# Optimization experiments

Measured on AMD Instinct MI355X. Metric: run time of the kernel, lower is better.

## Reference

```python
import jax, jax.numpy as jnp
from jax import lax
import numpy as np

N = 256          # HiPPO order
DT = 1.0 / 4096  # discretization step ~ 1/L
L = 4096         # sequence length
BATCH = 64


def _legt_transition(n):
    # LegT (translated Legendre) HiPPO transition matrices (continuous-time).
    Q = np.arange(n, dtype=np.float64)
    R = (2.0 * Q + 1.0) ** 0.5
    j, i = np.meshgrid(Q, Q)
    A = R[:, None] * np.where(i < j, (-1.0) ** (i - j), 1.0) * R[None, :]
    B = R[:, None]
    return -A, B


def _bilinear_discretize(A, B, dt):
    # scipy.signal.cont2discrete(..., method='bilinear')
    n = A.shape[0]
    I = np.eye(n)
    M = np.linalg.inv(I - (dt / 2.0) * A)
    Ad = M @ (I + (dt / 2.0) * A)
    Bd = (M @ B) * dt
    return Ad, Bd


def setup_inputs() -> dict:
    key = jax.random.key(0)
    A, B = _legt_transition(N)
    Ad, Bd = _bilinear_discretize(A, B, DT)
    inputs = jax.random.normal(key, (L, BATCH), dtype=jnp.float32)
    return {
        "inputs": inputs,
        "A": jnp.asarray(Ad, dtype=jnp.float32),          # (N, N)
        "B": jnp.asarray(Bd.squeeze(-1), dtype=jnp.float32),  # (N,)
    }


def reference(inputs, A, B):
    # inputs: (L, BATCH) -> output cs: (L, BATCH, N)
    u = inputs[..., None]  # (L, BATCH, 1)
    c0 = jnp.zeros((inputs.shape[1], A.shape[0]), dtype=inputs.dtype)  # (BATCH, N)

    def step(c, f):
        # c = F.linear(c, A) + B * f  ==  c @ A^T + B * f
        c = c @ A.T + B * f
        return c, c

    _, cs = lax.scan(step, c0, u)
    return cs
```

## Files before the change

### kernel.cpp

```cpp
#include <hip/hip_runtime.h>
#include <hip/hip_bf16.h>


#define MATF 65536

typedef __attribute__((ext_vector_type(8))) short short8;
typedef __attribute__((ext_vector_type(4))) float f32x4;

__device__ __forceinline__ unsigned short f2bf(float x) {
  union { __hip_bfloat16 h; unsigned short u; } cv;
  cv.h = __float2bfloat16(x);
  return cv.u;
}
__device__ __forceinline__ float bf2f(unsigned short u) {
  union { unsigned short u; __hip_bfloat16 h; } cv;
  cv.u = u;
  return __bfloat162float(cv.h);
}

__device__ __forceinline__ void load16_lds(const void* gsrc, void* ldst) {
  __builtin_amdgcn_global_load_lds(
      (const __attribute__((address_space(1))) unsigned int*)gsrc,
      (__attribute__((address_space(3))) unsigned int*)ldst,
      16, 0, 0);
}

__global__ __launch_bounds__(256) void gemm_nn_batch(
    const float* __restrict__ X, const float* __restrict__ Ys,
    float* __restrict__ Zs, int count)
{
  int g    = blockIdx.x >> 4;
  int tile = blockIdx.x & 15;
  if (g >= count) return;
  const float* Y = Ys + (size_t)g * MATF;
  float*       Z = Zs + (size_t)g * MATF;
  int tr = (tile >> 2) * 64;
  int tc = (tile & 3) * 64;

  __shared__ float As[64][33];
  __shared__ float Bs[32][65];
  int tid = threadIdx.x;
  int tx = tid & 15, ty = tid >> 4;
  float acc[4][4] = {};

  for (int k0 = 0; k0 < 256; k0 += 32) {
#pragma unroll
    for (int p = 0; p < 2; ++p) {
      int idx = tid + p * 256;
      int r = idx >> 3, c4 = (idx & 7) * 4;
      float4 v = *(const float4*)(X + (size_t)(tr + r) * 256 + k0 + c4);
      As[r][c4 + 0] = v.x; As[r][c4 + 1] = v.y; As[r][c4 + 2] = v.z; As[r][c4 + 3] = v.w;
    }
#pragma unroll
    for (int p = 0; p < 2; ++p) {
      int idx = tid + p * 256;
      int r = idx >> 4, c4 = (idx & 15) * 4;
      float4 v = *(const float4*)(Y + (size_t)(k0 + r) * 256 + tc + c4);
      Bs[r][c4 + 0] = v.x; Bs[r][c4 + 1] = v.y; Bs[r][c4 + 2] = v.z; Bs[r][c4 + 3] = v.w;
    }
    __syncthreads();
#pragma unroll
    for (int kk = 0; kk < 32; ++kk) {
      float a[4], b[4];
#pragma unroll
      for (int u = 0; u < 4; ++u) a[u] = As[ty * 4 + u][kk];
#pragma unroll
      for (int v = 0; v < 4; ++v) b[v] = Bs[kk][tx * 4 + v];
#pragma unroll
      for (int u = 0; u < 4; ++u)
#pragma unroll
        for (int v = 0; v < 4; ++v) acc[u][v] += a[u] * b[v];
    }
    __syncthreads();
  }
#pragma unroll
  for (int u = 0; u < 4; ++u)
#pragma unroll
    for (int v = 0; v < 4; ++v)
      Z[(size_t)(tr + ty * 4 + u) * 256 + tc + tx * 4 + v] = acc[u][v];
}

__global__ __launch_bounds__(256) void pow_first(
    const float* __restrict__ A, float* __restrict__ P)
{
  int bid = blockIdx.x, tid = threadIdx.x;
  if (bid >= 16) {
    int blk = bid - 16;
#pragma unroll
    for (int q = 0; q < 4; ++q) {
      int idx = blk * 1024 + q * 256 + tid;
      *(float4*)(P + (size_t)idx * 4) = *(const float4*)(A + (size_t)idx * 4);
    }
    return;
  }
  int tile = bid;
  int tr = (tile >> 2) * 64;
  int tc = (tile & 3) * 64;
  __shared__ float As[64][33];
  __shared__ float Bs[32][65];
  int tx = tid & 15, ty = tid >> 4;
  float acc[4][4] = {};
  for (int k0 = 0; k0 < 256; k0 += 32) {
#pragma unroll
    for (int p = 0; p < 2; ++p) {
      int idx = tid + p * 256;
      int r = idx >> 3, c4 = (idx & 7) * 4;
      float4 v = *(const float4*)(A + (size_t)(tr + r) * 256 + k0 + c4);
      As[r][c4 + 0] = v.x; As[r][c4 + 1] = v.y; As[r][c4 + 2] = v.z; As[r][c4 + 3] = v.w;
    }
#pragma unroll
    for (int p = 0; p < 2; ++p) {
      int idx = tid + p * 256;
      int r = idx >> 4, c4 = (idx & 15) * 4;
      float4 v = *(const float4*)(A + (size_t)(k0 + r) * 256 + tc + c4);
      Bs[r][c4 + 0] = v.x; Bs[r][c4 + 1] = v.y; Bs[r][c4 + 2] = v.z; Bs[r][c4 + 3] = v.w;
    }
    __syncthreads();
#pragma unroll
    for (int kk = 0; kk < 32; ++kk) {
      float a[4], b[4];
#pragma unroll
      for (int u = 0; u < 4; ++u) a[u] = As[ty * 4 + u][kk];
#pragma unroll
      for (int v = 0; v < 4; ++v) b[v] = Bs[kk][tx * 4 + v];
#pragma unroll
      for (int u = 0; u < 4; ++u)
#pragma unroll
        for (int v = 0; v < 4; ++v) acc[u][v] += a[u] * b[v];
    }
    __syncthreads();
  }
#pragma unroll
  for (int u = 0; u < 4; ++u)
#pragma unroll
    for (int v = 0; v < 4; ++v)
      P[(size_t)MATF + (size_t)(tr + ty * 4 + u) * 256 + tc + tx * 4 + v] = acc[u][v];
}

__global__ __launch_bounds__(256) void kv_kernel(
    const float* __restrict__ P, const float* __restrict__ Bv,
    float* __restrict__ Kv)
{
  int j = blockIdx.x;
  int n = threadIdx.x;
  __shared__ float bs[256];
  bs[n] = Bv[n];
  __syncthreads();
  if (j == 0) { Kv[n] = bs[n]; return; }
  const float* M = P + (size_t)(j - 1) * MATF;
  float acc = 0.f;
  for (int m = 0; m < 256; ++m) acc += M[(size_t)n * 256 + m] * bs[m];
  Kv[(size_t)j * 256 + n] = acc;
}

__global__ __launch_bounds__(256) void e_kernel(
    const float* __restrict__ in, const float* __restrict__ Kv,
    float* __restrict__ e)
{
  int k = blockIdx.x >> 6;
  int b = blockIdx.x & 63;
  int n = threadIdx.x;
  __shared__ float fs[64];
  if (n < 64) fs[n] = in[(size_t)(k * 64 + n) * 64 + b];
  __syncthreads();
  float acc = 0.f;
#pragma unroll
  for (int j = 0; j < 64; ++j) acc += Kv[(size_t)j * 256 + n] * fs[63 - j];
  e[((size_t)k * 256 + n) * 64 + b] = acc;
}

__global__ __launch_bounds__(256) void scan_round(
    const float* __restrict__ win, float* __restrict__ wout,
    const float* __restrict__ M, int d,
    float* __restrict__ MSdst,
    const float* __restrict__ P, const float* __restrict__ Kv,
    unsigned short* __restrict__ Gt, int gt_row0, int gt_off)
{
  __shared__ float As[64][33];
  __shared__ float Bs[32][65];
  int bid = blockIdx.x;
  int tid = threadIdx.x;

  if (bid >= gt_off) {
    int r2 = gt_row0 + (bid - gt_off);
    if (r2 >= 16384) return;
    int i = r2 >> 8, n = r2 & 255;
    unsigned short* dst = Gt + (size_t)r2 * 640;
    for (int c = tid; c < 320; c += 256) {
      float x;
      if (c < 64) x = (c <= i) ? Kv[(size_t)(i - c) * 256 + n] : 0.f;
      else        x = P[(size_t)i * MATF + (size_t)n * 256 + (c - 64)];
      unsigned short hi = f2bf(x);
      float lo = x - bf2f(hi);
      dst[c]       = hi;
      dst[320 + c] = f2bf(lo);
    }
    return;
  }
  if (bid >= 256) {
    int tile = bid - 256;
    int tr = (tile >> 2) * 64;
    int tc = (tile & 3) * 64;
    int tx = tid & 15, ty = tid >> 4;
    float acc[4][4] = {};
    for (int k0 = 0; k0 < 256; k0 += 32) {
#pragma unroll
      for (int p = 0; p < 2; ++p) {
        int idx = tid + p * 256;
        int r = idx >> 3, c4 = (idx & 7) * 4;
        float4 v = *(const float4*)(M + (size_t)(tr + r) * 256 + k0 + c4);
        As[r][c4 + 0] = v.x; As[r][c4 + 1] = v.y; As[r][c4 + 2] = v.z; As[r][c4 + 3] = v.w;
      }
#pragma unroll
      for (int p = 0; p < 2; ++p) {
        int idx = tid + p * 256;
        int r = idx >> 4, c4 = (idx & 15) * 4;
        float4 v = *(const float4*)(M + (size_t)(k0 + r) * 256 + tc + c4);
        Bs[r][c4 + 0] = v.x; Bs[r][c4 + 1] = v.y; Bs[r][c4 + 2] = v.z; Bs[r][c4 + 3] = v.w;
      }
      __syncthreads();
#pragma unroll
      for (int kk = 0; kk < 32; ++kk) {
        float a[4], b[4];
#pragma unroll
        for (int u = 0; u < 4; ++u) a[u] = As[ty * 4 + u][kk];
#pragma unroll
        for (int v = 0; v < 4; ++v) b[v] = Bs[kk][tx * 4 + v];
#pragma unroll
        for (int u = 0; u < 4; ++u)
#pragma unroll
          for (int v = 0; v < 4; ++v) acc[u][v] += a[u] * b[v];
      }
      __syncthreads();
    }
#pragma unroll
    for (int u = 0; u < 4; ++u)
#pragma unroll
      for (int v = 0; v < 4; ++v)
        MSdst[(size_t)(tr + ty * 4 + u) * 256 + tc + tx * 4 + v] = acc[u][v];
    return;
  }

  int k  = bid >> 2;
  int rt = bid & 3;
  const float* src = win  + (size_t)k * 16384;
  float*       dst = wout + (size_t)k * 16384;
  if (k < d) {
#pragma unroll
    for (int p = 0; p < 16; ++p) {
      int idx = rt * 4096 + p * 256 + tid;
      dst[idx] = src[idx];
    }
    return;
  }
  const float* v = win + (size_t)(k - d) * 16384;
  int tx = tid & 15, ty = tid >> 4;
  float acc[4][4] = {};
  for (int k0 = 0; k0 < 256; k0 += 32) {
#pragma unroll
    for (int p = 0; p < 2; ++p) {
      int idx = tid + p * 256;
      int r = idx >> 3, c4 = (idx & 7) * 4;
      float4 t4 = *(const float4*)(M + (size_t)(rt * 64 + r) * 256 + k0 + c4);
      As[r][c4 + 0] = t4.x; As[r][c4 + 1] = t4.y; As[r][c4 + 2] = t4.z; As[r][c4 + 3] = t4.w;
    }
#pragma unroll
    for (int p = 0; p < 2; ++p) {
      int idx = tid + p * 256;
      int r = idx >> 4, c4 = (idx & 15) * 4;
      float4 t4 = *(const float4*)(v + (size_t)(k0 + r) * 64 + c4);
      Bs[r][c4 + 0] = t4.x; Bs[r][c4 + 1] = t4.y; Bs[r][c4 + 2] = t4.z; Bs[r][c4 + 3] = t4.w;
    }
    __syncthreads();
#pragma unroll
    for (int kk = 0; kk < 32; ++kk) {
      float a[4], b[4];
#pragma unroll
      for (int u = 0; u < 4; ++u) a[u] = As[ty * 4 + u][kk];
#pragma unroll
      for (int v2 = 0; v2 < 4; ++v2) b[v2] = Bs[kk][tx * 4 + v2];
#pragma unroll
      for (int u = 0; u < 4; ++u)
#pragma unroll
        for (int v2 = 0; v2 < 4; ++v2) acc[u][v2] += a[u] * b[v2];
    }
    __syncthreads();
  }
#pragma unroll
  for (int u = 0; u < 4; ++u)
#pragma unroll
    for (int v2 = 0; v2 < 4; ++v2) {
      int idx = (rt * 64 + ty * 4 + u) * 64 + tx * 4 + v2;
      dst[idx] = src[idx] + acc[u][v2];
    }
}

__global__ __launch_bounds__(320) void build_ht(
    const float* __restrict__ in, const float* __restrict__ w,
    unsigned short* __restrict__ Ht)
{
  int row = blockIdx.x;
  int k = row >> 6, b = row & 63;
  int j = threadIdx.x;
  float x;
  if (j < 64) x = in[(size_t)(k * 64 + j) * 64 + b];
  else        x = (k > 0) ? w[((size_t)(k - 1) * 256 + (j - 64)) * 64 + b] : 0.f;
  unsigned short hi = f2bf(x);
  float lo = x - bf2f(hi);
  Ht[(size_t)row * 640 + j]       = hi;
  Ht[(size_t)row * 640 + 320 + j] = f2bf(lo);
}

__global__ __launch_bounds__(256) void out_gemm(
    const unsigned short* __restrict__ Ht,
    const unsigned short* __restrict__ Gt,
    float* __restrict__ out)
{
  __shared__ char smem[65536];

  int bid = blockIdx.x;
  int swz = (bid & 7) * 512 + (bid >> 3);
  int nt = swz >> 5;
  int mt = swz & 31;
  int mrow0 = mt * 128, nrow0 = nt * 128;

  int tid = threadIdx.x;
  int w = tid >> 6, l = tid & 63;
  int wm = w >> 1, wn = w & 1;

  auto stage = [&](const unsigned short* src, int row0, char* lds, int k0) {
#pragma unroll
    for (int it = 0; it < 4; ++it) {
      int L = it * 4096 + tid * 16;
      int row = L >> 7;
      int p = (L >> 4) & 7;
      int o = p ^ (row & 7);
      int h = o >> 2, q = o & 3;
      const void* g = src + (size_t)(row0 + row) * 640 + h * 320 + k0 + q * 8;
      void* dst = lds + (it * 4096 + w * 1024);
      load16_lds(g, dst);
    }
  };

  stage(Ht, mrow0, smem, 0);
  stage(Gt, nrow0, smem + 16384, 0);
  __syncthreads();

  f32x4 acc[4][4] = {};
  int rAbase = wm * 64 + (l & 15);
  int rBbase = wn * 64 + (l & 15);
  int qo = l >> 4;

  for (int ks = 0; ks < 10; ++ks) {
    char* cur = smem + (ks & 1) * 32768;
    if (ks < 9) {
      char* nxt = smem + ((ks + 1) & 1) * 32768;
      stage(Ht, mrow0, nxt, (ks + 1) * 32);
      stage(Gt, nrow0, nxt + 16384, (ks + 1) * 32);
    }
    char* Ab = cur;
    char* Bb = cur + 16384;
    short8 ah[4], al[4], bh[4], bl[4];
#pragma unroll
    for (int mf = 0; mf < 4; ++mf) {
      int r = rAbase + mf * 16;
      int ph = (qo)     ^ (r & 7);
      int pl = (4 + qo) ^ (r & 7);
      ah[mf] = *(const short8*)(Ab + r * 128 + ph * 16);
      al[mf] = *(const short8*)(Ab + r * 128 + pl * 16);
    }
#pragma unroll
    for (int nf = 0; nf < 4; ++nf) {
      int r = rBbase + nf * 16;
      int ph = (qo)     ^ (r & 7);
      int pl = (4 + qo) ^ (r & 7);
      bh[nf] = *(const short8*)(Bb + r * 128 + ph * 16);
      bl[nf] = *(const short8*)(Bb + r * 128 + pl * 16);
    }
#pragma unroll
    for (int mf = 0; mf < 4; ++mf)
#pragma unroll
      for (int nf = 0; nf < 4; ++nf) {
        acc[mf][nf] = __builtin_amdgcn_mfma_f32_16x16x32_bf16(ah[mf], bh[nf], acc[mf][nf], 0, 0, 0);
        acc[mf][nf] = __builtin_amdgcn_mfma_f32_16x16x32_bf16(ah[mf], bl[nf], acc[mf][nf], 0, 0, 0);
        acc[mf][nf] = __builtin_amdgcn_mfma_f32_16x16x32_bf16(al[mf], bh[nf], acc[mf][nf], 0, 0, 0);
      }
    __syncthreads();
  }

  int Mbase = mrow0 + wm * 64 + (l >> 4) * 4;
  int Nbase = nrow0 + wn * 64 + (l & 15);
#pragma unroll
  for (int mf = 0; mf < 4; ++mf)
#pragma unroll
    for (int nf = 0; nf < 4; ++nf)
#pragma unroll
      for (int r = 0; r < 4; ++r) {
        int Mrow = Mbase + mf * 16 + r;
        int Ncol = Nbase + nf * 16;
        int k = Mrow >> 6, b = Mrow & 63;
        int i = Ncol >> 8, n = Ncol & 255;
        out[((size_t)k * 4096 + (size_t)i * 64 + b) * 256 + n] = acc[mf][nf][r];
      }
}

extern "C" void kernel_launch(void* const* d_in, const int* in_sizes, int n_in,
                              void* d_out, int out_size, void* d_ws, size_t ws_size,
                              hipStream_t stream)
{
  const float* in = (const float*)d_in[0];
  const float* A  = (const float*)d_in[1];
  const float* Bv = (const float*)d_in[2];
  float* out = (float*)d_out;
  float* ws  = (float*)d_ws;

  float* P  = ws;
  float* Kv = P  + (size_t)64 * MATF;
  float* e  = Kv + (size_t)64 * 256;
  float* w2 = e  + (size_t)64 * 16384;
  float* MS = w2 + (size_t)64 * 16384;
  unsigned short* Ht = (unsigned short*)(MS + (size_t)2 * MATF);
  unsigned short* Gt = Ht + (size_t)4096 * 640;

  pow_first<<<dim3(32), dim3(256), 0, stream>>>(A, P);
  for (int m = 2; m <= 32; m <<= 1) {
    gemm_nn_batch<<<dim3(m * 16), dim3(256), 0, stream>>>(
        P + (size_t)(m - 1) * MATF, P, P + (size_t)m * MATF, m);
  }
  kv_kernel<<<dim3(64), dim3(256), 0, stream>>>(P, Bv, Kv);
  e_kernel<<<dim3(4096), dim3(256), 0, stream>>>(in, Kv, e);

  float* bufs[2] = {e, w2};
  for (int r = 0; r < 6; ++r) {
    const float* M = (r == 0) ? (P + (size_t)63 * MATF)
                              : (MS + (size_t)((r - 1) & 1) * MATF);
    float* MSdst = MS + (size_t)(r & 1) * MATF;
    int gt_row0 = r * 2731;
    int gt_cnt  = (r < 5) ? 2731 : (16384 - 5 * 2731);
    int gt_off  = (r < 5) ? 272 : 256;
    int grid    = gt_off + gt_cnt;
    scan_round<<<dim3(grid), dim3(256), 0, stream>>>(
        bufs[r & 1], bufs[(r + 1) & 1], M, 1 << r,
        MSdst, P, Kv, Gt, gt_row0, gt_off);
  }

  build_ht<<<dim3(4096), dim3(320), 0, stream>>>(in, e, Ht);

  out_gemm<<<dim3(4096), dim3(256), 0, stream>>>(Ht, Gt, out);
}
```

Baseline: 404.8 us.

## Enlarge output GEMM tile to 256x256 with 512 threads, single-buffered LDS

The output GEMM now gives each block a 256x256 tile on 8 waves (each wave does 128x64) instead of a 128x128 tile on 4 waves, with 1024 blocks instead of 4096. This raises operand reuse and cuts global re-reads of Ht and Gt. The LDS double buffer is dropped: the next k-slice is loaded after a barrier once compute finishes, so loads no longer overlap with MFMA work. Accumulator registers double to 8x4 fragments per wave, which may limit occupancy.

```diff
diff --git a/kernel.cpp b/kernel.cpp
--- a/kernel.cpp
+++ b/kernel.cpp
@@ -311,64 +311,50 @@
   Ht[(size_t)row * 640 + 320 + j] = f2bf(lo);
 }
 
-__global__ __launch_bounds__(256) void out_gemm(
+__global__ __launch_bounds__(512) void out_gemm(
     const unsigned short* __restrict__ Ht,
     const unsigned short* __restrict__ Gt,
     float* __restrict__ out)
 {
   __shared__ char smem[65536];
+  char* Ab = smem;
+  char* Bb = smem + 32768;
 
   int bid = blockIdx.x;
-  int swz = (bid & 7) * 512 + (bid >> 3);
-  int nt = swz >> 5;
-  int mt = swz & 31;
-  int mrow0 = mt * 128, nrow0 = nt * 128;
+  int swz = (bid & 7) * 128 + (bid >> 3);
+  int mt = swz >> 6;
+  int nt = swz & 63;
+  int mrow0 = mt * 256, nrow0 = nt * 256;
 
   int tid = threadIdx.x;
   int w = tid >> 6, l = tid & 63;
-  int wm = w >> 1, wn = w & 1;
+  int wm = w >> 2, wn = w & 3;
 
   auto stage = [&](const unsigned short* src, int row0, char* lds, int k0) {
 #pragma unroll
     for (int it = 0; it < 4; ++it) {
-      int L = it * 4096 + tid * 16;
+      int L = it * 8192 + tid * 16;
       int row = L >> 7;
       int p = (L >> 4) & 7;
       int o = p ^ (row & 7);
       int h = o >> 2, q = o & 3;
       const void* g = src + (size_t)(row0 + row) * 640 + h * 320 + k0 + q * 8;
-      void* dst = lds + (it * 4096 + w * 1024);
+      void* dst = lds + (it * 8192 + w * 1024);
       load16_lds(g, dst);
     }
   };
 
-  stage(Ht, mrow0, smem, 0);
-  stage(Gt, nrow0, smem + 16384, 0);
-  __syncthreads();
-
-  f32x4 acc[4][4] = {};
-  int rAbase = wm * 64 + (l & 15);
+  stage(Ht, mrow0, Ab, 0);
+  stage(Gt, nrow0, Bb, 0);
+
+  f32x4 acc[8][4] = {};
+  int rAbase = wm * 128 + (l & 15);
   int rBbase = wn * 64 + (l & 15);
   int qo = l >> 4;
 
   for (int ks = 0; ks < 10; ++ks) {
-    char* cur = smem + (ks & 1) * 32768;
-    if (ks < 9) {
-      char* nxt = smem + ((ks + 1) & 1) * 32768;
-      stage(Ht, mrow0, nxt, (ks + 1) * 32);
-      stage(Gt, nrow0, nxt + 16384, (ks + 1) * 32);
-    }
-    char* Ab = cur;
-    char* Bb = cur + 16384;
-    short8 ah[4], al[4], bh[4], bl[4];
-#pragma unroll
-    for (int mf = 0; mf < 4; ++mf) {
-      int r = rAbase + mf * 16;
-      int ph = (qo)     ^ (r & 7);
-      int pl = (4 + qo) ^ (r & 7);
-      ah[mf] = *(const short8*)(Ab + r * 128 + ph * 16);
-      al[mf] = *(const short8*)(Ab + r * 128 + pl * 16);
-    }
+    __syncthreads();
+    short8 bh[4], bl[4];
 #pragma unroll
     for (int nf = 0; nf < 4; ++nf) {
       int r = rBbase + nf * 16;
@@ -378,20 +364,30 @@
       bl[nf] = *(const short8*)(Bb + r * 128 + pl * 16);
     }
 #pragma unroll
-    for (int mf = 0; mf < 4; ++mf)
+    for (int mf = 0; mf < 8; ++mf) {
+      int r = rAbase + mf * 16;
+      int ph = (qo)     ^ (r & 7);
+      int pl = (4 + qo) ^ (r & 7);
+      short8 ah = *(const short8*)(Ab + r * 128 + ph * 16);
+      short8 al = *(const short8*)(Ab + r * 128 + pl * 16);
 #pragma unroll
       for (int nf = 0; nf < 4; ++nf) {
-        acc[mf][nf] = __builtin_amdgcn_mfma_f32_16x16x32_bf16(ah[mf], bh[nf], acc[mf][nf], 0, 0, 0);
-        acc[mf][nf] = __builtin_amdgcn_mfma_f32_16x16x32_bf16(ah[mf], bl[nf], acc[mf][nf], 0, 0, 0);
-        acc[mf][nf] = __builtin_amdgcn_mfma_f32_16x16x32_bf16(al[mf], bh[nf], acc[mf][nf], 0, 0, 0);
+        acc[mf][nf] = __builtin_amdgcn_mfma_f32_16x16x32_bf16(ah, bh[nf], acc[mf][nf], 0, 0, 0);
+        acc[mf][nf] = __builtin_amdgcn_mfma_f32_16x16x32_bf16(ah, bl[nf], acc[mf][nf], 0, 0, 0);
+        acc[mf][nf] = __builtin_amdgcn_mfma_f32_16x16x32_bf16(al, bh[nf], acc[mf][nf], 0, 0, 0);
       }
-    __syncthreads();
-  }
-
-  int Mbase = mrow0 + wm * 64 + (l >> 4) * 4;
+    }
+    __syncthreads();
+    if (ks < 9) {
+      stage(Ht, mrow0, Ab, (ks + 1) * 32);
+      stage(Gt, nrow0, Bb, (ks + 1) * 32);
+    }
+  }
+
+  int Mbase = mrow0 + wm * 128 + (l >> 4) * 4;
   int Nbase = nrow0 + wn * 64 + (l & 15);
 #pragma unroll
-  for (int mf = 0; mf < 4; ++mf)
+  for (int mf = 0; mf < 8; ++mf)
 #pragma unroll
     for (int nf = 0; nf < 4; ++nf)
 #pragma unroll
@@ -446,5 +442,5 @@
 
   build_ht<<<dim3(4096), dim3(320), 0, stream>>>(in, e, Ht);
 
-  out_gemm<<<dim3(4096), dim3(256), 0, stream>>>(Ht, Gt, out);
-}
+  out_gemm<<<dim3(1024), dim3(512), 0, stream>>>(Ht, Gt, out);
+}
```

After: 384.8 us (median of 3 runs). -4.9%, faster.
